# Kernel tuning notes

Measured on AMD Instinct MI355X. Metric: run time of the kernel, lower is better.

## Reference

```python
import jax, jax.numpy as jnp
import numpy as np

N_HEADS = 8
N_HIDDEN = 16  # out_features 128 / 8 heads
NEG_SLOPE = 0.2


def setup_inputs() -> dict:
    key = jax.random.key(0)
    k_h, k_adj, k_wl, k_wr, k_a = jax.random.split(key, 5)
    N, IN_F = 1024, 200
    OUT_F = N_HEADS * N_HIDDEN
    h = jax.random.normal(k_h, (1, N, IN_F), dtype=jnp.float32)
    adj = jax.random.randint(k_adj, (1, N, N), 0, 2, dtype=jnp.int32)
    # guarantee self-loops so no softmax row is fully masked
    adj = adj.at[0, jnp.arange(N), jnp.arange(N)].set(1)
    s_in = 1.0 / np.sqrt(IN_F)
    s_hid = 1.0 / np.sqrt(N_HIDDEN)
    W_l = jax.random.uniform(k_wl, (IN_F, OUT_F), jnp.float32, -s_in, s_in)
    W_r = jax.random.uniform(k_wr, (IN_F, OUT_F), jnp.float32, -s_in, s_in)
    attn_w = jax.random.uniform(k_a, (N_HIDDEN,), jnp.float32, -s_hid, s_hid)
    return {"h": h, "adj_mat": adj, "W_l": W_l, "W_r": W_r, "attn_w": attn_w}


def reference(h, adj_mat, W_l, W_r, attn_w):
    # h: [1, N, in_f]  (batch must be 1, as in the torch module)
    N = h.shape[1]
    x = h[0]                                   # [N, in_f]
    g_l = (x @ W_l).reshape(N, N_HEADS, N_HIDDEN)   # [N, H, F]
    g_r = (x @ W_r).reshape(N, N_HEADS, N_HIDDEN)   # [N, H, F]
    # g_sum[i, j, h, f] = g_r[i] + g_l[j]  (matches repeat/repeat_interleave)
    g_sum = g_r[:, None, :, :] + g_l[None, :, :, :]       # [N, N, H, F]
    e = jnp.einsum('ijhf,f->ijh',
                   jax.nn.leaky_relu(g_sum, NEG_SLOPE), attn_w)  # [N, N, H]
    mask = (adj_mat[0] != 0)[:, :, None]                  # [N, N, 1]
    e = jnp.where(mask, e, -jnp.inf)
    a = jax.nn.softmax(e, axis=1)                         # softmax over j
    # dropout is identity at inference
    out = jnp.einsum('ijh,jhf->ihf', a, g_r)              # [N, H, F]
    return out.reshape(1, N, N_HEADS * N_HIDDEN)
```

## Files before the change

### kernel.cpp

```cpp
#include <hip/hip_runtime.h>

#define NH 8
#define NF 16
#define NNODE 1024
#define INF_F 200
#define OUTF 128
#define IT 8
#define JS 16
#define JCH 64
#define ESTR (JCH + 2)
#define NEG_INF (-__builtin_huge_valf())

__global__ __launch_bounds__(256) void proj_kernel(
        const float* __restrict__ x,
        const float* __restrict__ Wl,
        const float* __restrict__ Wr,
        float* __restrict__ gl,
        float* __restrict__ gr) {
    __shared__ float xs[8 * INF_F];
    const float* __restrict__ W = blockIdx.y ? Wr : Wl;
    float* __restrict__ g = blockIdx.y ? gr : gl;
    const int i0 = blockIdx.x * 8;
    const int tid = threadIdx.x;

    {
        const float4* src = (const float4*)(x + i0 * INF_F);
        float4* dst = (float4*)xs;
        for (int t = tid; t < (8 * INF_F) / 4; t += 256) dst[t] = src[t];
    }
    __syncthreads();

    const int c = tid & 127;
    const int r0 = (tid >> 7) * 4;
    float acc[4] = {0.f, 0.f, 0.f, 0.f};
#pragma unroll 4
    for (int k = 0; k < INF_F; ++k) {
        const float w = W[k * OUTF + c];
#pragma unroll
        for (int r = 0; r < 4; ++r)
            acc[r] = fmaf(xs[(r0 + r) * INF_F + k], w, acc[r]);
    }
#pragma unroll
    for (int r = 0; r < 4; ++r)
        g[(i0 + r0 + r) * OUTF + c] = acc[r];
}

__global__ __launch_bounds__(512, 8) void gat_partial(
        const float* __restrict__ gl,
        const float* __restrict__ gr,
        const int* __restrict__ adj,
        const float* __restrict__ attn_w,
        float* __restrict__ outp,
        float* __restrict__ ps) {
    __shared__ float gri[IT][OUTF];
    __shared__ float p_lds[NH][IT][ESTR];

    const int bid = blockIdx.x;
    const int itile = bid >> 4;
    const int js = bid & 15;
    const int i0 = itile * IT;
    const int jbase = js * JCH;
    const int tid = threadIdx.x;
    const int h = tid >> 6;
    const int lane = tid & 63;

    *(float2*)((float*)gri + tid * 2) = *(const float2*)(gr + i0 * OUTF + tid * 2);
    __syncthreads();

    float w[NF];
#pragma unroll
    for (int f = 0; f < NF; ++f) w[f] = attn_w[f];

    {
        const int row = jbase + lane;
        float glr[NF];
        {
            const float4* gp = (const float4*)(gl + row * OUTF + h * NF);
            float4 g0 = gp[0], g1 = gp[1], g2 = gp[2], g3 = gp[3];
            glr[0]=g0.x; glr[1]=g0.y; glr[2]=g0.z; glr[3]=g0.w;
            glr[4]=g1.x; glr[5]=g1.y; glr[6]=g1.z; glr[7]=g1.w;
            glr[8]=g2.x; glr[9]=g2.y; glr[10]=g2.z; glr[11]=g2.w;
            glr[12]=g3.x; glr[13]=g3.y; glr[14]=g3.z; glr[15]=g3.w;
        }
#pragma unroll
        for (int i = 0; i < IT; ++i) {
            const float4* ap = (const float4*)(&gri[i][h * NF]);
            const float4 a0 = ap[0], a1 = ap[1], a2 = ap[2], a3 = ap[3];
            const float ga[NF] = {a0.x,a0.y,a0.z,a0.w, a1.x,a1.y,a1.z,a1.w,
                                  a2.x,a2.y,a2.z,a2.w, a3.x,a3.y,a3.z,a3.w};
            float e = 0.f;
#pragma unroll
            for (int f = 0; f < NF; ++f) {
                float v = ga[f] + glr[f];
                v = fmaxf(v, 0.2f * v);
                e = fmaf(v, w[f], e);
            }
            const int msk = adj[(i0 + i) * NNODE + row];
            p_lds[h][i][lane] = msk ? __expf(e) : 0.f;
        }
    }
    __syncthreads();

    {
        const int iq = lane >> 3;
        const int fq = (lane >> 1) & 3;
        const int jh = lane & 1;
        const float* pr = &p_lds[h][iq][jh * 32];
        const float* grb = gr + (jbase + jh * 32) * OUTF + h * NF + fq * 4;
        float4 acc = {0.f, 0.f, 0.f, 0.f};
        float den = 0.f;
#pragma unroll 8
        for (int t = 0; t < 32; ++t) {
            const float p = pr[t];
            const float4 g = *(const float4*)(grb + t * OUTF);
            acc.x = fmaf(p, g.x, acc.x);
            acc.y = fmaf(p, g.y, acc.y);
            acc.z = fmaf(p, g.z, acc.z);
            acc.w = fmaf(p, g.w, acc.w);
            den += p;
        }
        acc.x += __shfl_xor(acc.x, 1, 64);
        acc.y += __shfl_xor(acc.y, 1, 64);
        acc.z += __shfl_xor(acc.z, 1, 64);
        acc.w += __shfl_xor(acc.w, 1, 64);
        den   += __shfl_xor(den,   1, 64);
        if (jh == 0) {
            *(float4*)(outp + js * NNODE * OUTF + (i0 + iq) * OUTF + h * NF + fq * 4) = acc;
            if (fq == 0)
                ps[js * NNODE * NH + (i0 + iq) * NH + h] = den;
        }
    }
}

__global__ __launch_bounds__(256) void gat_reduce(
        const float* __restrict__ outp,
        const float* __restrict__ ps,
        float* __restrict__ out) {
    const int t = blockIdx.x * 256 + threadIdx.x;
    const int i = t >> 7;
    const int c = t & 127;
    const int h = c >> 4;
    float num = 0.f, den = 0.f;
#pragma unroll
    for (int s = 0; s < JS; ++s) {
        num += outp[s * NNODE * OUTF + i * OUTF + c];
        den += ps[s * NNODE * NH + i * NH + h];
    }
    out[t] = num / den;
}

extern "C" void kernel_launch(void* const* d_in, const int* in_sizes, int n_in,
                              void* d_out, int out_size, void* d_ws, size_t ws_size,
                              hipStream_t stream) {
    const float* h   = (const float*)d_in[0];
    const int*   adj = (const int*)d_in[1];
    const float* Wl  = (const float*)d_in[2];
    const float* Wr  = (const float*)d_in[3];
    const float* aw  = (const float*)d_in[4];
    float* out = (float*)d_out;

    float* gl   = (float*)d_ws;
    float* gr   = gl + NNODE * OUTF;
    float* outp = gr + NNODE * OUTF;
    float* ps   = outp + JS * NNODE * OUTF;

    proj_kernel<<<dim3(128, 2), 256, 0, stream>>>(h, Wl, Wr, gl, gr);
    gat_partial<<<dim3((NNODE / IT) * JS), 512, 0, stream>>>(gl, gr, adj, aw, outp, ps);
    gat_reduce<<<dim3(NNODE * OUTF / 256), 256, 0, stream>>>(outp, ps, out);
}
```

Before: 122.6 us.

## Double i-tile in GAT partial kernel, drop LDS staging and split-j shuffle

Raises the i-tile from 8 to 16 rows per block, so each block reuses its loaded gl rows and gr chunk across twice as many target nodes, and halves the block count. gr rows are now read straight from global (uniform per wavefront) instead of being staged in LDS with an extra barrier. Each thread now covers all 64 j values with two accumulators instead of splitting j across lanes and combining with a shuffle. The launch-bounds occupancy hint drops to 4. Risks are lower occupancy, fewer blocks, and a longer serial loop per thread.

```diff
diff --git a/kernel.cpp b/kernel.cpp
--- a/kernel.cpp
+++ b/kernel.cpp
@@ -5,11 +5,22 @@
 #define NNODE 1024
 #define INF_F 200
 #define OUTF 128
-#define IT 8
+#define IT 16
 #define JS 16
 #define JCH 64
 #define ESTR (JCH + 2)
-#define NEG_INF (-__builtin_huge_valf())
+
+__device__ __forceinline__ float dot_lrelu4(float4 a, float4 g, float4 w, float acc) {
+    float v0 = a.x + g.x; v0 = fmaxf(v0, 0.2f * v0);
+    float v1 = a.y + g.y; v1 = fmaxf(v1, 0.2f * v1);
+    float v2 = a.z + g.z; v2 = fmaxf(v2, 0.2f * v2);
+    float v3 = a.w + g.w; v3 = fmaxf(v3, 0.2f * v3);
+    acc = fmaf(v0, w.x, acc);
+    acc = fmaf(v1, w.y, acc);
+    acc = fmaf(v2, w.z, acc);
+    acc = fmaf(v3, w.w, acc);
+    return acc;
+}
 
 __global__ __launch_bounds__(256) void proj_kernel(
         const float* __restrict__ x,
@@ -45,14 +56,13 @@
         g[(i0 + r0 + r) * OUTF + c] = acc[r];
 }
 
-__global__ __launch_bounds__(512, 8) void gat_partial(
+__global__ __launch_bounds__(512, 4) void gat_partial(
         const float* __restrict__ gl,
         const float* __restrict__ gr,
         const int* __restrict__ adj,
         const float* __restrict__ attn_w,
         float* __restrict__ outp,
         float* __restrict__ ps) {
-    __shared__ float gri[IT][OUTF];
     __shared__ float p_lds[NH][IT][ESTR];
 
     const int bid = blockIdx.x;
@@ -61,74 +71,61 @@
     const int i0 = itile * IT;
     const int jbase = js * JCH;
     const int tid = threadIdx.x;
-    const int h = tid >> 6;
+    const int h = __builtin_amdgcn_readfirstlane(tid >> 6);
     const int lane = tid & 63;
 
-    *(float2*)((float*)gri + tid * 2) = *(const float2*)(gr + i0 * OUTF + tid * 2);
-    __syncthreads();
-
-    float w[NF];
-#pragma unroll
-    for (int f = 0; f < NF; ++f) w[f] = attn_w[f];
+    const float4* wp = (const float4*)attn_w;
+    const float4 W0 = wp[0], W1 = wp[1], W2 = wp[2], W3 = wp[3];
 
     {
         const int row = jbase + lane;
-        float glr[NF];
-        {
-            const float4* gp = (const float4*)(gl + row * OUTF + h * NF);
-            float4 g0 = gp[0], g1 = gp[1], g2 = gp[2], g3 = gp[3];
-            glr[0]=g0.x; glr[1]=g0.y; glr[2]=g0.z; glr[3]=g0.w;
-            glr[4]=g1.x; glr[5]=g1.y; glr[6]=g1.z; glr[7]=g1.w;
-            glr[8]=g2.x; glr[9]=g2.y; glr[10]=g2.z; glr[11]=g2.w;
-            glr[12]=g3.x; glr[13]=g3.y; glr[14]=g3.z; glr[15]=g3.w;
-        }
+        const float4* gp = (const float4*)(gl + (size_t)row * OUTF + h * NF);
+        const float4 G0 = gp[0], G1 = gp[1], G2 = gp[2], G3 = gp[3];
+        const int* __restrict__ arow = adj + (size_t)i0 * NNODE + row;
 #pragma unroll
         for (int i = 0; i < IT; ++i) {
-            const float4* ap = (const float4*)(&gri[i][h * NF]);
-            const float4 a0 = ap[0], a1 = ap[1], a2 = ap[2], a3 = ap[3];
-            const float ga[NF] = {a0.x,a0.y,a0.z,a0.w, a1.x,a1.y,a1.z,a1.w,
-                                  a2.x,a2.y,a2.z,a2.w, a3.x,a3.y,a3.z,a3.w};
+            const float4* ap = (const float4*)(gr + (size_t)(i0 + i) * OUTF + h * NF);
+            const float4 A0 = ap[0], A1 = ap[1], A2 = ap[2], A3 = ap[3];
             float e = 0.f;
-#pragma unroll
-            for (int f = 0; f < NF; ++f) {
-                float v = ga[f] + glr[f];
-                v = fmaxf(v, 0.2f * v);
-                e = fmaf(v, w[f], e);
-            }
-            const int msk = adj[(i0 + i) * NNODE + row];
+            e = dot_lrelu4(A0, G0, W0, e);
+            e = dot_lrelu4(A1, G1, W1, e);
+            e = dot_lrelu4(A2, G2, W2, e);
+            e = dot_lrelu4(A3, G3, W3, e);
+            const int msk = arow[i * NNODE];
             p_lds[h][i][lane] = msk ? __expf(e) : 0.f;
         }
     }
     __syncthreads();
 
     {
-        const int iq = lane >> 3;
-        const int fq = (lane >> 1) & 3;
-        const int jh = lane & 1;
-        const float* pr = &p_lds[h][iq][jh * 32];
-        const float* grb = gr + (jbase + jh * 32) * OUTF + h * NF + fq * 4;
-        float4 acc = {0.f, 0.f, 0.f, 0.f};
-        float den = 0.f;
+        const int iq = lane >> 2;
+        const int fq = lane & 3;
+        const float* pr = &p_lds[h][iq][0];
+        const float* grb = gr + (size_t)jbase * OUTF + h * NF + fq * 4;
+        float4 acc0 = {0.f, 0.f, 0.f, 0.f}, acc1 = {0.f, 0.f, 0.f, 0.f};
+        float den0 = 0.f, den1 = 0.f;
 #pragma unroll 8
-        for (int t = 0; t < 32; ++t) {
-            const float p = pr[t];
-            const float4 g = *(const float4*)(grb + t * OUTF);
-            acc.x = fmaf(p, g.x, acc.x);
-            acc.y = fmaf(p, g.y, acc.y);
-            acc.z = fmaf(p, g.z, acc.z);
-            acc.w = fmaf(p, g.w, acc.w);
-            den += p;
+        for (int j = 0; j < JCH; j += 2) {
+            const float pa = pr[j];
+            const float pb = pr[j + 1];
+            const float4 ga = *(const float4*)(grb + (size_t)j * OUTF);
+            const float4 gb = *(const float4*)(grb + (size_t)(j + 1) * OUTF);
+            acc0.x = fmaf(pa, ga.x, acc0.x);
+            acc0.y = fmaf(pa, ga.y, acc0.y);
+            acc0.z = fmaf(pa, ga.z, acc0.z);
+            acc0.w = fmaf(pa, ga.w, acc0.w);
+            den0 += pa;
+            acc1.x = fmaf(pb, gb.x, acc1.x);
+            acc1.y = fmaf(pb, gb.y, acc1.y);
+            acc1.z = fmaf(pb, gb.z, acc1.z);
+            acc1.w = fmaf(pb, gb.w, acc1.w);
+            den1 += pb;
         }
-        acc.x += __shfl_xor(acc.x, 1, 64);
-        acc.y += __shfl_xor(acc.y, 1, 64);
-        acc.z += __shfl_xor(acc.z, 1, 64);
-        acc.w += __shfl_xor(acc.w, 1, 64);
-        den   += __shfl_xor(den,   1, 64);
-        if (jh == 0) {
-            *(float4*)(outp + js * NNODE * OUTF + (i0 + iq) * OUTF + h * NF + fq * 4) = acc;
-            if (fq == 0)
-                ps[js * NNODE * NH + (i0 + iq) * NH + h] = den;
-        }
+        acc0.x += acc1.x; acc0.y += acc1.y; acc0.z += acc1.z; acc0.w += acc1.w;
+        const float den = den0 + den1;
+        *(float4*)(outp + (size_t)js * NNODE * OUTF + (size_t)(i0 + iq) * OUTF + h * NF + fq * 4) = acc0;
+        if (fq == 0)
+            ps[(size_t)js * NNODE * NH + (i0 + iq) * NH + h] = den;
     }
 }
 
@@ -143,8 +140,8 @@
     float num = 0.f, den = 0.f;
 #pragma unroll
     for (int s = 0; s < JS; ++s) {
-        num += outp[s * NNODE * OUTF + i * OUTF + c];
-        den += ps[s * NNODE * NH + i * NH + h];
+        num += outp[(size_t)s * NNODE * OUTF + i * OUTF + c];
+        den += ps[(size_t)s * NNODE * NH + i * NH + h];
     }
     out[t] = num / den;
 }
@@ -162,7 +159,7 @@
     float* gl   = (float*)d_ws;
     float* gr   = gl + NNODE * OUTF;
     float* outp = gr + NNODE * OUTF;
-    float* ps   = outp + JS * NNODE * OUTF;
+    float* ps   = outp + (size_t)JS * NNODE * OUTF;
 
     proj_kernel<<<dim3(128, 2), 256, 0, stream>>>(h, Wl, Wr, gl, gr);
     gat_partial<<<dim3((NNODE / IT) * JS), 512, 0, stream>>>(gl, gr, adj, aw, outp, ps);
```

Result: faster. 110.8 us (-9.6%).
